# Optimization experiments

Measured on AMD Instinct MI355X. Metric: run time of the kernel, lower is better.

## Reference

```python
import math
import jax, jax.numpy as jnp
import numpy as np

RADIUS = 1.5
NUM_R = 4
NUM_THETA = 8
C_IN = 8
C_OUT = 8
EPS = 1e-9


def _bilinear_sample_zeros(ker, grid):
    """torch.F.grid_sample(mode='bilinear', padding_mode='zeros', align_corners=False)
    ker:  [C, H, W] (shared across batch, torch expands it)
    grid: [B, M, N, 2] with grid[...,0]=x (W axis), grid[...,1]=y (H axis), in [-1,1]
    returns [C, B, M, N]
    """
    C, H, W = ker.shape
    x, y = grid[..., 0], grid[..., 1]
    ix = ((x + 1.0) * W - 1.0) * 0.5   # unnormalize, align_corners=False
    iy = ((y + 1.0) * H - 1.0) * 0.5
    x0 = jnp.floor(ix)
    y0 = jnp.floor(iy)
    wx = ix - x0
    wy = iy - y0

    def corner(xi, yi, w):
        valid = (xi >= 0) & (xi <= W - 1) & (yi >= 0) & (yi <= H - 1)
        xc = jnp.clip(xi, 0, W - 1).astype(jnp.int32)
        yc = jnp.clip(yi, 0, H - 1).astype(jnp.int32)
        v = ker[:, yc, xc]                        # [C, B, M, N]
        return v * (w * valid)[None]

    return (corner(x0, y0, (1 - wx) * (1 - wy))
            + corner(x0 + 1, y0, wx * (1 - wy))
            + corner(x0, y0 + 1, (1 - wx) * wy)
            + corner(x0 + 1, y0 + 1, wx * wy))


def setup_inputs() -> dict:
    key = jax.random.key(0)
    ks = jax.random.split(key, 4)
    B, M, N = 2, 384, 384
    field = jax.random.normal(ks[0], (B, N, 2), dtype=jnp.float32)
    center = jax.random.normal(ks[1], (B, M, 2), dtype=jnp.float32)
    field_feat = jax.random.normal(ks[2], (B, N, C_IN, 2), dtype=jnp.float32)
    field_mask = jnp.ones((B, N, 1), dtype=jnp.float32)
    kernel = jax.random.normal(ks[3], (C_OUT, C_IN, NUM_R, NUM_THETA, 2, 2), dtype=jnp.float32)
    return {"field": field, "center": center, "field_feat": field_feat,
            "field_mask": field_mask, "kernel": kernel}


def reference(field, center, field_feat, field_mask, kernel):
    B, M = center.shape[0], center.shape[1]
    N = field.shape[1]
    # relative positions, scaled to kernel support
    rel = (field[:, None, :, :] - center[:, :, None, :]) / RADIUS   # [B,M,N,2]
    # polar coordinates
    r = jnp.sqrt(rel[..., 0] ** 2 + rel[..., 1] ** 2 + EPS)          # [B,M,N]
    nonzero = ~((rel[..., 0] == 0.0) & (rel[..., 1] == 0.0))
    theta = jnp.where(nonzero, jnp.arctan2(rel[..., 1], rel[..., 0]), 0.0)
    # grid_sample normalized coords: x over radius axis, y over (padded) theta axis
    gx = 2.0 * r - 1.0
    gy = theta * (1.0 / math.pi) * (NUM_THETA / (NUM_THETA + 2.0))
    grid = jnp.stack([gx, gy], axis=-1)                              # [B,M,N,2]
    # kernel [co,ci,r,th,2,2] -> [co,ci,2,2,r,th] -> [C,r,th], circular-pad theta
    ker = kernel.transpose(0, 1, 4, 5, 2, 3).reshape(-1, NUM_R, NUM_THETA)
    ker = jnp.concatenate([ker[..., -1:], ker, ker[..., :1]], axis=-1)  # [C,r,th+2]
    ker = ker.transpose(0, 2, 1)                                     # [C, th+2, r]
    kof = _bilinear_sample_zeros(ker, grid)                          # [C,B,M,N]
    kof = kof.transpose(1, 2, 3, 0).reshape(B, M, N, C_OUT, C_IN, 2, 2)
    # attention: relu((1 - |rel|^2)^3) masked by field_mask
    att = jax.nn.relu((1.0 - jnp.sum(rel ** 2, axis=-1)) ** 3)[..., None]  # [B,M,N,1]
    att = att * field_mask[:, None]                                  # [B,M,N,1]
    psi = jnp.sum(att, axis=2)[..., 0]                               # [B,M]
    psi = jnp.where(psi == 0.0, 1.0, psi)[:, :, None, None]          # [B,M,1,1]
    aff = field_feat[:, None] * att[..., None]                       # [B,M,N,ci,2]
    out = jnp.einsum('bmnoiyx,bmnix->bmoy', kof, aff)                # [B,M,co,2]
    return out / psi
```

## Files before the change

### kernel.cpp

```cpp
#include <hip/hip_runtime.h>
#include <math.h>

#define B_ 2
#define M_ 384
#define N_ 384
#define NTY 10
#define NSLOT 640
#define NW 4
#define BS 256

__device__ __forceinline__ float fast_atan2f(float y, float x) {
  float ax = fabsf(x), ay = fabsf(y);
  float mx = fmaxf(ax, ay), mn = fminf(ax, ay);
  float a = mn * __builtin_amdgcn_rcpf(mx);
  if (mx == 0.f) a = 0.f;
  float s = a * a;
  float p = -0.0117212f;
  p = fmaf(p, s, 0.05265332f);
  p = fmaf(p, s, -0.11643287f);
  p = fmaf(p, s, 0.19354346f);
  p = fmaf(p, s, -0.33262347f);
  p = fmaf(p, s, 0.99997726f);
  float r = p * a;
  if (ay > ax) r = 1.57079632679f - r;
  if (x < 0.f) r = 3.14159265359f - r;
  return (y < 0.f) ? -r : r;
}

__global__ __launch_bounds__(BS) void equiconv_kernel(
    const float* __restrict__ field,
    const float* __restrict__ center,
    const float* __restrict__ feat,
    const float* __restrict__ mask,
    const float* __restrict__ kern,
    float* __restrict__ out) {
  __shared__ float4 sMeta[N_];
  __shared__ float4 sG4[N_ * 4];
  __shared__ float  sS4[NW][NSLOT];
  __shared__ float  sS[NSLOT];
  __shared__ float  sPartial[16][17];
  __shared__ float  sPsi[NW];
  __shared__ int    sCnt;

  int t = threadIdx.x;
  int bm = blockIdx.x;
  int b = bm / M_;

  if (t == 0) sCnt = 0;
  if (t < NW) sPsi[t] = 0.f;
  __syncthreads();

  float cx = center[bm * 2 + 0];
  float cy = center[bm * 2 + 1];
  const float invR = 1.0f / 1.5f;
  const float fourpi = 4.0f / 3.14159265358979323846f;
  float psi_acc = 0.f;

  for (int n = t; n < N_; n += BS) {
    int fn = b * N_ + n;
    float2 fxy = ((const float2*)field)[fn];
    float msk = mask[fn];
    const float4* fp = (const float4*)(feat + fn * 16);
    float4 f0 = fp[0], f1 = fp[1], f2 = fp[2], f3 = fp[3];

    float rx = (fxy.x - cx) * invR;
    float ry = (fxy.y - cy) * invR;
    float r2 = rx * rx + ry * ry;
    float onem = 1.f - r2;
    float attr = onem * onem * onem;
    float att = attr * msk;

    float r = sqrtf(r2 + 1e-9f);
    float theta = fast_atan2f(ry, rx);
    float ix = 4.f * r - 0.5f;
    float iy = theta * fourpi + 4.5f;
    float x0f = floorf(ix), y0f = floorf(iy);
    int x0 = (int)x0f, y0 = (int)y0f;

    if (attr > 0.f && att != 0.f) {
      psi_acc += att;
      int a = atomicAdd(&sCnt, 1);
      sMeta[a] = make_float4(
          __int_as_float((x0 + 1) | (y0 << 8)), ix - x0f, iy - y0f, 0.f);
      float4* gp = &sG4[a * 4];
      f0.x *= att; f0.y *= att; f0.z *= att; f0.w *= att;
      f1.x *= att; f1.y *= att; f1.z *= att; f1.w *= att;
      f2.x *= att; f2.y *= att; f2.z *= att; f2.w *= att;
      f3.x *= att; f3.y *= att; f3.z *= att; f3.w *= att;
      gp[0] = f0; gp[1] = f1; gp[2] = f2; gp[3] = f3;
    }
  }

#pragma unroll
  for (int off = 32; off > 0; off >>= 1)
    psi_acc += __shfl_xor(psi_acc, off, 64);
  if ((t & 63) == 0) sPsi[t >> 6] = psi_acc;
  __syncthreads();
  int cnt = sCnt;

  int f   = t & 15;
  int xr4 = (t >> 4) & 3;
  int w   = t >> 6;
  const float* sG = (const float*)sG4;

  float acc[NTY];
#pragma unroll
  for (int k = 0; k < NTY; ++k) acc[k] = 0.f;

  int chunk = (cnt + NW - 1) / NW;
  int a0 = w * chunk;
  int a1 = min(a0 + chunk, cnt);
#pragma unroll 2
  for (int a = a0; a < a1; ++a) {
    float4 md = sMeta[a];
    float g = sG[a * 16 + f];
    int meta = __float_as_int(md.x);
    int x0 = (meta & 255) - 1;
    int y0 = meta >> 8;
    float wx1 = md.y, wy1 = md.z;
    float ux = (xr4 == x0) ? (1.f - wx1) : ((xr4 == x0 + 1) ? wx1 : 0.f);
    float ug = ux * g;
    float wy0 = 1.f - wy1;
#pragma unroll
    for (int k = 0; k < NTY; ++k) {
      float vy = (k == y0) ? wy0 : ((k == y0 + 1) ? wy1 : 0.f);
      acc[k] = fmaf(vy, ug, acc[k]);
    }
  }
#pragma unroll
  for (int k = 0; k < NTY; ++k)
    sS4[w][(k * 4 + xr4) * 16 + f] = acc[k];
  __syncthreads();

  for (int s = t; s < NSLOT; s += BS) {
    float v = sS4[0][s] + sS4[1][s] + sS4[2][s] + sS4[3][s];
    sS[s] = v;
  }
  __syncthreads();

  {
    int oy = t & 15, grp = t >> 4;
    int o = oy >> 1, y = oy & 1;
    float cacc = 0.f;
    for (int c = grp; c < 40; c += 16) {
      int ty = c >> 2, cxr = c & 3;
      int th = (ty + 7) & 7;
      const float* sp = &sS[c * 16];
#pragma unroll
      for (int ff = 0; ff < 16; ++ff) {
        int i = ff >> 1, x = ff & 1;
        int idx = ((((o * 8 + i) * 4 + cxr) * 8 + th) * 2 + y) * 2 + x;
        cacc = fmaf(kern[idx], sp[ff], cacc);
      }
    }
    sPartial[grp][oy] = cacc;
  }
  __syncthreads();

  if (t < 16) {
    float sum = 0.f;
#pragma unroll
    for (int gg = 0; gg < 16; ++gg) sum += sPartial[gg][t];
    float psi = sPsi[0] + sPsi[1] + sPsi[2] + sPsi[3];
    if (psi == 0.f) psi = 1.f;
    out[bm * 16 + t] = sum / psi;
  }
}

extern "C" void kernel_launch(void* const* d_in, const int* in_sizes, int n_in,
                              void* d_out, int out_size, void* d_ws, size_t ws_size,
                              hipStream_t stream) {
  (void)in_sizes; (void)n_in; (void)out_size; (void)d_ws; (void)ws_size;
  const float* field  = (const float*)d_in[0];
  const float* center = (const float*)d_in[1];
  const float* feat   = (const float*)d_in[2];
  const float* mask   = (const float*)d_in[3];
  const float* kern   = (const float*)d_in[4];
  float* out = (float*)d_out;

  equiconv_kernel<<<dim3(B_ * M_), dim3(BS), 0, stream>>>(
      field, center, feat, mask, kern, out);
}
```

Before: 82.89 us.

## Split per-center work into four single-wave blocks plus a separate finish kernel

The single 256-thread block per output center becomes four 64-thread blocks, each handling a quarter of the field points. Compaction uses a wave ballot instead of a shared atomic counter. Features are read straight from global memory inside the accumulation loop rather than staged in shared memory. Partial sums and psi go to workspace, and a second kernel reduces them and applies the kernel weights. This removes block-level syncs and shared-memory staging and raises block count, at the cost of an extra launch and workspace round trip (about 7.9 MB written and read).

```diff
diff --git a/kernel.cpp b/kernel.cpp
--- a/kernel.cpp
+++ b/kernel.cpp
@@ -6,8 +6,8 @@
 #define N_ 384
 #define NTY 10
 #define NSLOT 640
-#define NW 4
-#define BS 256
+#define QN 96
+#define NQ 4
 
 __device__ __forceinline__ float fast_atan2f(float y, float x) {
   float ax = fabsf(x), ay = fabsf(y);
@@ -27,98 +27,75 @@
   return (y < 0.f) ? -r : r;
 }
 
-__global__ __launch_bounds__(BS) void equiconv_kernel(
+__global__ __launch_bounds__(64) void accum_kernel(
     const float* __restrict__ field,
     const float* __restrict__ center,
     const float* __restrict__ feat,
     const float* __restrict__ mask,
-    const float* __restrict__ kern,
-    float* __restrict__ out) {
-  __shared__ float4 sMeta[N_];
-  __shared__ float4 sG4[N_ * 4];
-  __shared__ float  sS4[NW][NSLOT];
-  __shared__ float  sS[NSLOT];
-  __shared__ float  sPartial[16][17];
-  __shared__ float  sPsi[NW];
-  __shared__ int    sCnt;
+    float* __restrict__ wsS,
+    float* __restrict__ wsPsi) {
+  __shared__ float4 sMeta[QN];
 
   int t = threadIdx.x;
-  int bm = blockIdx.x;
+  int blk = blockIdx.x;
+  int bm = blk >> 2, q = blk & 3;
   int b = bm / M_;
-
-  if (t == 0) sCnt = 0;
-  if (t < NW) sPsi[t] = 0.f;
-  __syncthreads();
 
   float cx = center[bm * 2 + 0];
   float cy = center[bm * 2 + 1];
   const float invR = 1.0f / 1.5f;
   const float fourpi = 4.0f / 3.14159265358979323846f;
-  float psi_acc = 0.f;
+  float psi = 0.f;
+  int cnt = 0;
 
-  for (int n = t; n < N_; n += BS) {
+#pragma unroll
+  for (int r = 0; r < 2; ++r) {
+    int off = r * 64 + t;
+    bool elig = off < QN;
+    int n = q * QN + (elig ? off : 0);
     int fn = b * N_ + n;
     float2 fxy = ((const float2*)field)[fn];
     float msk = mask[fn];
-    const float4* fp = (const float4*)(feat + fn * 16);
-    float4 f0 = fp[0], f1 = fp[1], f2 = fp[2], f3 = fp[3];
-
     float rx = (fxy.x - cx) * invR;
     float ry = (fxy.y - cy) * invR;
     float r2 = rx * rx + ry * ry;
     float onem = 1.f - r2;
     float attr = onem * onem * onem;
     float att = attr * msk;
-
-    float r = sqrtf(r2 + 1e-9f);
+    float rr = sqrtf(r2 + 1e-9f);
     float theta = fast_atan2f(ry, rx);
-    float ix = 4.f * r - 0.5f;
+    float ix = 4.f * rr - 0.5f;
     float iy = theta * fourpi + 4.5f;
     float x0f = floorf(ix), y0f = floorf(iy);
     int x0 = (int)x0f, y0 = (int)y0f;
 
-    if (attr > 0.f && att != 0.f) {
-      psi_acc += att;
-      int a = atomicAdd(&sCnt, 1);
-      sMeta[a] = make_float4(
-          __int_as_float((x0 + 1) | (y0 << 8)), ix - x0f, iy - y0f, 0.f);
-      float4* gp = &sG4[a * 4];
-      f0.x *= att; f0.y *= att; f0.z *= att; f0.w *= att;
-      f1.x *= att; f1.y *= att; f1.z *= att; f1.w *= att;
-      f2.x *= att; f2.y *= att; f2.z *= att; f2.w *= att;
-      f3.x *= att; f3.y *= att; f3.z *= att; f3.w *= att;
-      gp[0] = f0; gp[1] = f1; gp[2] = f2; gp[3] = f3;
+    bool pred = elig && (attr > 0.f) && (att != 0.f);
+    unsigned long long bmask = __ballot(pred);
+    int pos = cnt + __popcll(bmask & ((1ull << t) - 1ull));
+    if (pred) {
+      int meta = fn | ((x0 + 1) << 12) | (y0 << 16);
+      sMeta[pos] = make_float4(__int_as_float(meta), att, ix - x0f, iy - y0f);
+      psi += att;
     }
+    cnt += __popcll(bmask);
   }
 
-#pragma unroll
-  for (int off = 32; off > 0; off >>= 1)
-    psi_acc += __shfl_xor(psi_acc, off, 64);
-  if ((t & 63) == 0) sPsi[t >> 6] = psi_acc;
-  __syncthreads();
-  int cnt = sCnt;
-
-  int f   = t & 15;
-  int xr4 = (t >> 4) & 3;
-  int w   = t >> 6;
-  const float* sG = (const float*)sG4;
-
+  int f  = t & 15;
+  int xr = t >> 4;
   float acc[NTY];
 #pragma unroll
   for (int k = 0; k < NTY; ++k) acc[k] = 0.f;
 
-  int chunk = (cnt + NW - 1) / NW;
-  int a0 = w * chunk;
-  int a1 = min(a0 + chunk, cnt);
 #pragma unroll 2
-  for (int a = a0; a < a1; ++a) {
+  for (int a = 0; a < cnt; ++a) {
     float4 md = sMeta[a];
-    float g = sG[a * 16 + f];
     int meta = __float_as_int(md.x);
-    int x0 = (meta & 255) - 1;
-    int y0 = meta >> 8;
-    float wx1 = md.y, wy1 = md.z;
-    float ux = (xr4 == x0) ? (1.f - wx1) : ((xr4 == x0 + 1) ? wx1 : 0.f);
+    int fn = meta & 0xFFF;
+    float g = feat[fn * 16 + f] * md.y;
+    int x0 = ((meta >> 12) & 7) - 1;
+    int y0 = (meta >> 16) & 15;
+    float wx1 = md.z, wy1 = md.w;
+    float ux = (xr == x0) ? (1.f - wx1) : ((xr == x0 + 1) ? wx1 : 0.f);
     float ug = ux * g;
     float wy0 = 1.f - wy1;
 #pragma unroll
@@ -127,41 +104,56 @@
       acc[k] = fmaf(vy, ug, acc[k]);
     }
   }
+
+  float* Sp = wsS + blk * NSLOT;
 #pragma unroll
-  for (int k = 0; k < NTY; ++k)
-    sS4[w][(k * 4 + xr4) * 16 + f] = acc[k];
+  for (int k = 0; k < NTY; ++k) Sp[k * 64 + t] = acc[k];
+
+#pragma unroll
+  for (int off = 32; off > 0; off >>= 1) psi += __shfl_xor(psi, off, 64);
+  if (t == 0) wsPsi[blk] = psi;
+}
+
+__global__ __launch_bounds__(256) void finish_kernel(
+    const float* __restrict__ wsS,
+    const float* __restrict__ wsPsi,
+    const float* __restrict__ kern,
+    float* __restrict__ out) {
+  __shared__ float sS[NSLOT];
+  __shared__ float sPartial[16][17];
+  __shared__ float sPsi4[NQ];
+
+  int t = threadIdx.x;
+  int bm = blockIdx.x;
+
+  if (t < NQ) sPsi4[t] = wsPsi[bm * NQ + t];
+  const float* p = wsS + bm * NQ * NSLOT;
+  for (int s = t; s < NSLOT; s += 256)
+    sS[s] = p[s] + p[NSLOT + s] + p[2 * NSLOT + s] + p[3 * NSLOT + s];
   __syncthreads();
 
-  for (int s = t; s < NSLOT; s += BS) {
-    float v = sS4[0][s] + sS4[1][s] + sS4[2][s] + sS4[3][s];
-    sS[s] = v;
+  int oy = t & 15, grp = t >> 4;
+  int o = oy >> 1, y = oy & 1;
+  float cacc = 0.f;
+  for (int c = grp; c < 40; c += 16) {
+    int ty = c >> 2, cxr = c & 3;
+    int th = (ty + 7) & 7;
+    const float* sp = &sS[c * 16];
+#pragma unroll
+    for (int ff = 0; ff < 16; ++ff) {
+      int i = ff >> 1, x = ff & 1;
+      int idx = ((((o * 8 + i) * 4 + cxr) * 8 + th) * 2 + y) * 2 + x;
+      cacc = fmaf(kern[idx], sp[ff], cacc);
+    }
   }
-  __syncthreads();
-
-  {
-    int oy = t & 15, grp = t >> 4;
-    int o = oy >> 1, y = oy & 1;
-    float cacc = 0.f;
-    for (int c = grp; c < 40; c += 16) {
-      int ty = c >> 2, cxr = c & 3;
-      int th = (ty + 7) & 7;
-      const float* sp = &sS[c * 16];
-#pragma unroll
-      for (int ff = 0; ff < 16; ++ff) {
-        int i = ff >> 1, x = ff & 1;
-        int idx = ((((o * 8 + i) * 4 + cxr) * 8 + th) * 2 + y) * 2 + x;
-        cacc = fmaf(kern[idx], sp[ff], cacc);
-      }
-    }
-    sPartial[grp][oy] = cacc;
-  }
+  sPartial[grp][oy] = cacc;
   __syncthreads();
 
   if (t < 16) {
     float sum = 0.f;
 #pragma unroll
     for (int gg = 0; gg < 16; ++gg) sum += sPartial[gg][t];
-    float psi = sPsi[0] + sPsi[1] + sPsi[2] + sPsi[3];
+    float psi = sPsi4[0] + sPsi4[1] + sPsi4[2] + sPsi4[3];
     if (psi == 0.f) psi = 1.f;
     out[bm * 16 + t] = sum / psi;
   }
@@ -170,14 +162,18 @@
 extern "C" void kernel_launch(void* const* d_in, const int* in_sizes, int n_in,
                               void* d_out, int out_size, void* d_ws, size_t ws_size,
                               hipStream_t stream) {
-  (void)in_sizes; (void)n_in; (void)out_size; (void)d_ws; (void)ws_size;
+  (void)in_sizes; (void)n_in; (void)out_size; (void)ws_size;
   const float* field  = (const float*)d_in[0];
   const float* center = (const float*)d_in[1];
   const float* feat   = (const float*)d_in[2];
   const float* mask   = (const float*)d_in[3];
   const float* kern   = (const float*)d_in[4];
   float* out = (float*)d_out;
+  float* wsS = (float*)d_ws;
+  float* wsPsi = wsS + (B_ * M_ * NQ) * NSLOT;
 
-  equiconv_kernel<<<dim3(B_ * M_), dim3(BS), 0, stream>>>(
-      field, center, feat, mask, kern, out);
+  accum_kernel<<<dim3(B_ * M_ * NQ), dim3(64), 0, stream>>>(
+      field, center, feat, mask, wsS, wsPsi);
+  finish_kernel<<<dim3(B_ * M_), dim3(256), 0, stream>>>(
+      wsS, wsPsi, kern, out);
 }
```

New measurement: 93.02 us. 1.12x slower.

## Replace shared atomic compaction with per-wave ballot compaction and wave-local lists

Applied to the files above, without the earlier changes.

Each wave now owns a fixed 96-point slice of the field and compacts its active points into a private shared-memory list using ballot and popcount, in place of a block-wide atomic counter. This removes the shared atomics and the two block barriers around the compaction phase, so each wave goes straight from compaction to accumulation over its own list. The trade-off is load imbalance: work per wave now depends on how many active points fall in its slice, whereas before the compacted list was split evenly across waves. The second unrolled iteration also runs with only half its lanes eligible.

```diff
diff --git a/kernel.cpp b/kernel.cpp
--- a/kernel.cpp
+++ b/kernel.cpp
@@ -6,8 +6,7 @@
 #define N_ 384
 #define NTY 10
 #define NSLOT 640
-#define NW 4
-#define BS 256
+#define WN 96
 
 __device__ __forceinline__ float fast_atan2f(float y, float x) {
   float ax = fabsf(x), ay = fabsf(y);
@@ -27,36 +26,38 @@
   return (y < 0.f) ? -r : r;
 }
 
-__global__ __launch_bounds__(BS) void equiconv_kernel(
+__global__ __launch_bounds__(256) void equiconv_kernel(
     const float* __restrict__ field,
     const float* __restrict__ center,
     const float* __restrict__ feat,
     const float* __restrict__ mask,
     const float* __restrict__ kern,
     float* __restrict__ out) {
-  __shared__ float4 sMeta[N_];
-  __shared__ float4 sG4[N_ * 4];
-  __shared__ float  sS4[NW][NSLOT];
+  __shared__ float4 sMeta[4][WN];
+  __shared__ float4 sG4[4][WN * 4];
+  __shared__ float  sS4[4][NSLOT];
   __shared__ float  sS[NSLOT];
   __shared__ float  sPartial[16][17];
-  __shared__ float  sPsi[NW];
-  __shared__ int    sCnt;
+  __shared__ float  sPsi[4];
 
   int t = threadIdx.x;
+  int lane = t & 63;
+  int w = t >> 6;
   int bm = blockIdx.x;
   int b = bm / M_;
-
-  if (t == 0) sCnt = 0;
-  if (t < NW) sPsi[t] = 0.f;
-  __syncthreads();
 
   float cx = center[bm * 2 + 0];
   float cy = center[bm * 2 + 1];
   const float invR = 1.0f / 1.5f;
   const float fourpi = 4.0f / 3.14159265358979323846f;
-  float psi_acc = 0.f;
+  float psi = 0.f;
+  int cnt = 0;
 
-  for (int n = t; n < N_; n += BS) {
+#pragma unroll
+  for (int r = 0; r < 2; ++r) {
+    int off = r * 64 + lane;
+    bool elig = off < WN;
+    int n = w * WN + (elig ? off : 0);
     int fn = b * N_ + n;
     float2 fxy = ((const float2*)field)[fn];
     float msk = mask[fn];
@@ -70,55 +71,51 @@
     float attr = onem * onem * onem;
     float att = attr * msk;
 
-    float r = sqrtf(r2 + 1e-9f);
+    float rr = sqrtf(r2 + 1e-9f);
     float theta = fast_atan2f(ry, rx);
-    float ix = 4.f * r - 0.5f;
+    float ix = 4.f * rr - 0.5f;
     float iy = theta * fourpi + 4.5f;
     float x0f = floorf(ix), y0f = floorf(iy);
     int x0 = (int)x0f, y0 = (int)y0f;
 
-    if (attr > 0.f && att != 0.f) {
-      psi_acc += att;
-      int a = atomicAdd(&sCnt, 1);
-      sMeta[a] = make_float4(
+    bool pred = elig && (attr > 0.f) && (att != 0.f);
+    unsigned long long bmask = __ballot(pred);
+    int pos = cnt + __popcll(bmask & ((1ull << lane) - 1ull));
+    if (pred) {
+      psi += att;
+      sMeta[w][pos] = make_float4(
           __int_as_float((x0 + 1) | (y0 << 8)), ix - x0f, iy - y0f, 0.f);
-      float4* gp = &sG4[a * 4];
+      float4* gp = &sG4[w][pos * 4];
       f0.x *= att; f0.y *= att; f0.z *= att; f0.w *= att;
       f1.x *= att; f1.y *= att; f1.z *= att; f1.w *= att;
       f2.x *= att; f2.y *= att; f2.z *= att; f2.w *= att;
       f3.x *= att; f3.y *= att; f3.z *= att; f3.w *= att;
       gp[0] = f0; gp[1] = f1; gp[2] = f2; gp[3] = f3;
     }
+    cnt += __popcll(bmask);
   }
 
 #pragma unroll
-  for (int off = 32; off > 0; off >>= 1)
-    psi_acc += __shfl_xor(psi_acc, off, 64);
-  if ((t & 63) == 0) sPsi[t >> 6] = psi_acc;
-  __syncthreads();
-  int cnt = sCnt;
+  for (int off = 32; off > 0; off >>= 1) psi += __shfl_xor(psi, off, 64);
+  if (lane == 0) sPsi[w] = psi;
 
-  int f   = t & 15;
-  int xr4 = (t >> 4) & 3;
-  int w   = t >> 6;
-  const float* sG = (const float*)sG4;
+  int f  = lane & 15;
+  int xr = lane >> 4;
+  const float* sGf = (const float*)&sG4[w][0];
 
   float acc[NTY];
 #pragma unroll
   for (int k = 0; k < NTY; ++k) acc[k] = 0.f;
 
-  int chunk = (cnt + NW - 1) / NW;
-  int a0 = w * chunk;
-  int a1 = min(a0 + chunk, cnt);
 #pragma unroll 2
-  for (int a = a0; a < a1; ++a) {
-    float4 md = sMeta[a];
-    float g = sG[a * 16 + f];
+  for (int a = 0; a < cnt; ++a) {
+    float4 md = sMeta[w][a];
+    float g = sGf[a * 16 + f];
     int meta = __float_as_int(md.x);
     int x0 = (meta & 255) - 1;
     int y0 = meta >> 8;
     float wx1 = md.y, wy1 = md.z;
-    float ux = (xr4 == x0) ? (1.f - wx1) : ((xr4 == x0 + 1) ? wx1 : 0.f);
+    float ux = (xr == x0) ? (1.f - wx1) : ((xr == x0 + 1) ? wx1 : 0.f);
     float ug = ux * g;
     float wy0 = 1.f - wy1;
 #pragma unroll
@@ -129,13 +126,11 @@
   }
 #pragma unroll
   for (int k = 0; k < NTY; ++k)
-    sS4[w][(k * 4 + xr4) * 16 + f] = acc[k];
+    sS4[w][k * 64 + lane] = acc[k];
   __syncthreads();
 
-  for (int s = t; s < NSLOT; s += BS) {
-    float v = sS4[0][s] + sS4[1][s] + sS4[2][s] + sS4[3][s];
-    sS[s] = v;
-  }
+  for (int s = t; s < NSLOT; s += 256)
+    sS[s] = sS4[0][s] + sS4[1][s] + sS4[2][s] + sS4[3][s];
   __syncthreads();
 
   {
@@ -161,9 +156,9 @@
     float sum = 0.f;
 #pragma unroll
     for (int gg = 0; gg < 16; ++gg) sum += sPartial[gg][t];
-    float psi = sPsi[0] + sPsi[1] + sPsi[2] + sPsi[3];
-    if (psi == 0.f) psi = 1.f;
-    out[bm * 16 + t] = sum / psi;
+    float p4 = sPsi[0] + sPsi[1] + sPsi[2] + sPsi[3];
+    if (p4 == 0.f) p4 = 1.f;
+    out[bm * 16 + t] = sum / p4;
   }
 }
 
@@ -178,6 +173,6 @@
   const float* kern   = (const float*)d_in[4];
   float* out = (float*)d_out;
 
-  equiconv_kernel<<<dim3(B_ * M_), dim3(BS), 0, stream>>>(
+  equiconv_kernel<<<dim3(B_ * M_), dim3(256), 0, stream>>>(
       field, center, feat, mask, kern, out);
 }
```

Result: no change. 83.37 us (+0.6%).
